# Optimization experiments

Hardware: AMD Instinct MI355X
Metric: run time of the kernel (lower is better)

The kernel has to match this reference:

```python
import jax, jax.numpy as jnp
import numpy as np

H_SIZE = 64  # height_pad == width_pad == 64 (power of 2, no padding needed)


def _hadamard(n):
    H = np.array([[1.0]], dtype=np.float32)
    while H.shape[0] < n:
        H = np.block([[H, H], [H, -H]])
    return jnp.asarray(H)


def setup_inputs() -> dict:
    key = jax.random.key(0)
    k1, k2, k3, k4 = jax.random.split(key, 4)
    B, C_in, C_out, P = 32, 256, 256, 2
    x = jax.random.normal(k1, (B, C_in, H_SIZE, H_SIZE), dtype=jnp.float32)
    v = jax.random.uniform(k2, (P, H_SIZE, H_SIZE), dtype=jnp.float32)
    W = jax.random.normal(k3, (P, C_out, C_in), dtype=jnp.float32) * (1.0 / np.sqrt(C_in))
    T = jax.random.uniform(k4, (P, H_SIZE, H_SIZE), dtype=jnp.float32) * 0.1
    return {"x": x, "v": v, "W": W, "T": T}


def reference(x, v, W, T):
    n = H_SIZE
    H = _hadamard(n)  # symmetric, H @ H = n * I
    # 2D WHT: apply along width then height
    f1 = jnp.einsum('bchw,wk->bchk', x, H)
    f2 = jnp.einsum('bchw,hk->bckw', f1, H)
    # per-pod: scale, 1x1 conv, soft-threshold
    f3 = v[:, None, None, :, :] * f2[None]                 # (p,b,c,h,w)
    f4 = jnp.einsum('poc,pbchw->pbohw', W, f3)             # 1x1 conv, no bias
    f5 = jnp.sign(f4) * jnp.maximum(jnp.abs(f4) - T[:, None, None, :, :], 0.0)
    f6 = f5.sum(axis=0)                                     # sum over pods
    # inverse 2D WHT (H^{-1} = H / n)
    f7 = jnp.einsum('bchw,wk->bchk', f6, H) / n
    f8 = jnp.einsum('bchw,hk->bckw', f7, H) / n
    return f8 + x  # residual
```

## Files before the change

### kernel.cpp

```cpp
#include <hip/hip_runtime.h>
#include <stdint.h>


typedef __attribute__((ext_vector_type(4))) float f32x4_t;
typedef __attribute__((ext_vector_type(8))) __bf16 bf16x8_t;
typedef __attribute__((ext_vector_type(8))) unsigned short u16x8_t;
typedef __attribute__((ext_vector_type(4))) unsigned short u16x4_t;

__device__ __forceinline__ float bf2f(unsigned short u) {
  union { unsigned int i; float f; } x; x.i = ((unsigned int)u) << 16; return x.f;
}
__device__ __forceinline__ unsigned short f2bf(float f) {
  union { float f; unsigned int i; } x; x.f = f;
  unsigned int i = x.i;
  return (unsigned short)((i + 0x7FFFu + ((i >> 16) & 1u)) >> 16);
}
__device__ __forceinline__ unsigned short f2bf_t(float f) {
  union { float f; unsigned int i; } x; x.f = f;
  return (unsigned short)(x.i >> 16);
}
__device__ __forceinline__ size_t Faddr(size_t f) {
  return ((f >> 12) << 13) + 4096 + (f & 4095);
}

__global__ __launch_bounds__(512) void k_fwd(const float* __restrict__ x,
                                             unsigned short* __restrict__ obuf) {
  __shared__ unsigned short smem[36864];
  int tid = threadIdx.x;
  int lane = tid & 63, wave = tid >> 6;
  int quad = lane >> 4, l15 = lane & 15;
  int cg = blockIdx.x, b = blockIdx.y;
  size_t img = (size_t)b * 256 + cg * 8 + wave;
  unsigned short* T1t = smem + wave * 4608;

  const float* xim = x + img * 4096;
#pragma unroll
  for (int l = 0; l < 16; l++) {
    int e = (l * 64 + lane) * 4;
    f32x4_t sv = *(const f32x4_t*)(xim + e);
    u16x4_t u;
#pragma unroll
    for (int j = 0; j < 4; j++) u[j] = f2bf_t(sv[j]);
    int row = e >> 6, col = e & 63;
    *(u16x4_t*)&T1t[row * 72 + col] = u;
  }

  bf16x8_t hf[2][4];
#pragma unroll
  for (int kc = 0; kc < 2; kc++)
#pragma unroll
    for (int t = 0; t < 4; t++) {
      bf16x8_t h;
#pragma unroll
      for (int j = 0; j < 8; j++) {
        int k = kc * 32 + quad * 8 + j, n = t * 16 + l15;
        h[j] = (__builtin_popcount(k & n) & 1) ? (__bf16)-1.0f : (__bf16)1.0f;
      }
      hf[kc][t] = h;
    }

  bf16x8_t xa[4][2];
#pragma unroll
  for (int mt = 0; mt < 4; mt++)
#pragma unroll
    for (int kc = 0; kc < 2; kc++)
      xa[mt][kc] = *(const bf16x8_t*)&T1t[(mt * 16 + l15) * 72 + kc * 32 + quad * 8];

#pragma unroll
  for (int nt = 0; nt < 4; nt++) {
    f32x4_t a1c[4];
#pragma unroll
    for (int mt = 0; mt < 4; mt++) a1c[mt] = (f32x4_t){0.f, 0.f, 0.f, 0.f};
#pragma unroll
    for (int kc = 0; kc < 2; kc++)
#pragma unroll
      for (int mt = 0; mt < 4; mt++)
        a1c[mt] = __builtin_amdgcn_mfma_f32_16x16x32_bf16(xa[mt][kc], hf[kc][nt], a1c[mt], 0, 0, 0);
#pragma unroll
    for (int mt = 0; mt < 4; mt++) {
      u16x4_t t4;
#pragma unroll
      for (int r = 0; r < 4; r++) t4[r] = f2bf_t(a1c[mt][r]);
      *(u16x4_t*)&T1t[(nt * 16 + l15) * 72 + mt * 16 + quad * 4] = t4;
    }
  }

  f32x4_t acc[4][4];
#pragma unroll
  for (int mt = 0; mt < 4; mt++)
#pragma unroll
    for (int nt = 0; nt < 4; nt++) acc[mt][nt] = (f32x4_t){0.f, 0.f, 0.f, 0.f};
#pragma unroll
  for (int kc = 0; kc < 2; kc++)
#pragma unroll
    for (int nt = 0; nt < 4; nt++) {
      bf16x8_t bfr = *(bf16x8_t*)&T1t[(nt * 16 + l15) * 72 + kc * 32 + quad * 8];
#pragma unroll
      for (int mt = 0; mt < 4; mt++)
        acc[mt][nt] = __builtin_amdgcn_mfma_f32_16x16x32_bf16(hf[kc][mt], bfr, acc[mt][nt], 0, 0, 0);
    }

  __syncthreads();
#pragma unroll
  for (int mt = 0; mt < 4; mt++)
#pragma unroll
    for (int nt = 0; nt < 4; nt++)
#pragma unroll
      for (int r = 0; r < 4; r++) {
        int pos = (mt * 16 + quad * 4 + r) * 64 + nt * 16 + l15;
        smem[pos * 8 + wave] = f2bf(acc[mt][nt][r]);
      }
  __syncthreads();
  size_t fbase = ((size_t)b * 32 + cg) * 4096;
#pragma unroll
  for (int i = 0; i < 8; i++) {
    int pos = i * 512 + tid;
    u16x8_t vch = *(u16x8_t*)&smem[pos * 8];
    *(u16x8_t*)(obuf + Faddr((fbase + pos) * 8)) = vch;
  }
}

__global__ __launch_bounds__(256) void k_gemm(const float* __restrict__ Wf,
                                              const float* __restrict__ vv,
                                              const float* __restrict__ TT,
                                              unsigned short* __restrict__ obuf) {
  __shared__ unsigned short smem2[24576];
  unsigned short* Alds = smem2;
  int tid = threadIdx.x;
  int lane = tid & 63, wave = tid >> 6;
  int quad = lane >> 4, l15 = lane & 15;
  int wm = wave & 1, wn = wave >> 1;
  int n0 = blockIdx.x * 128;
  int m0 = blockIdx.y * 128;
  int b  = blockIdx.z;

  f32x4_t acc[4][4];
#pragma unroll
  for (int mt = 0; mt < 4; mt++)
#pragma unroll
    for (int nt = 0; nt < 4; nt++) acc[mt][nt] = (f32x4_t){0.f, 0.f, 0.f, 0.f};

  auto issueB = [&](int ks, int buf) {
    unsigned short* Bl = smem2 + 8192 + buf * 8192;
#pragma unroll
    for (int i = 0; i < 4; i++) {
      int idx = i * 256 + tid;
      int r = idx & 127, cch = idx >> 7;
      size_t f = (((size_t)b * 32 + ks * 8 + cch) * 4096 + n0 + r) * 8;
      const unsigned short* src = obuf + Faddr(f);
      __builtin_amdgcn_global_load_lds(
          (const __attribute__((address_space(1))) void*)src,
          (__attribute__((address_space(3))) void*)(Bl + idx * 8), 16, 0, 0);
    }
  };
  auto loadA = [&](int ks, f32x4_t (&ar)[4][2]) {
    int k0 = ks * 64;
#pragma unroll
    for (int i = 0; i < 4; i++) {
      int idx = i * 256 + tid;
      int r = idx >> 3, cch = idx & 7;
      int m = m0 + r;
      const float* wp = Wf + ((m & 1) << 16) + ((m >> 1) << 8) + k0 + cch * 8;
      ar[i][0] = *(const f32x4_t*)wp;
      ar[i][1] = *(const f32x4_t*)(wp + 4);
    }
  };
  auto writeA = [&](f32x4_t (&ar)[4][2]) {
#pragma unroll
    for (int i = 0; i < 4; i++) {
      int idx = i * 256 + tid;
      int r = idx >> 3, cch = idx & 7;
      u16x8_t u;
#pragma unroll
      for (int j = 0; j < 4; j++) { u[j] = f2bf_t(ar[i][0][j]); u[4 + j] = f2bf_t(ar[i][1][j]); }
      *(u16x8_t*)&Alds[cch * 1024 + r * 8] = u;
    }
  };

  f32x4_t areg[4][2];
  issueB(0, 0);
  loadA(0, areg);
  writeA(areg);
  __syncthreads();

  int kbuf = 0;
  for (int ks = 0; ks < 4; ++ks) {
    if (ks < 3) {
      issueB(ks + 1, kbuf ^ 1);
      loadA(ks + 1, areg);
    }
    unsigned short* Bl = smem2 + 8192 + kbuf * 8192;
#pragma unroll
    for (int kk = 0; kk < 2; ++kk) {
      int ch = kk * 4 + quad;
      bf16x8_t af[4], bfr[4];
#pragma unroll
      for (int mt = 0; mt < 4; mt++)
        af[mt] = *(const bf16x8_t*)&Alds[ch * 1024 + (wm * 64 + mt * 16 + l15) * 8];
#pragma unroll
      for (int nt = 0; nt < 4; nt++)
        bfr[nt] = *(const bf16x8_t*)&Bl[ch * 1024 + (wn * 64 + nt * 16 + l15) * 8];
#pragma unroll
      for (int mt = 0; mt < 4; mt++)
#pragma unroll
        for (int nt = 0; nt < 4; nt++)
          acc[mt][nt] = __builtin_amdgcn_mfma_f32_16x16x32_bf16(af[mt], bfr[nt], acc[mt][nt], 0, 0, 0);
    }
    __syncthreads();
    if (ks < 3) {
      writeA(areg);
      __syncthreads();
    }
    kbuf ^= 1;
  }

#pragma unroll
  for (int nt = 0; nt < 4; nt++) {
    int posl = wn * 64 + nt * 16 + l15;
    int pos = n0 + posl;
    float v0 = vv[pos], v1 = vv[4096 + pos];
    float t0 = TT[pos], t1 = TT[4096 + pos];
#pragma unroll
    for (int mt = 0; mt < 4; mt++)
#pragma unroll
      for (int rp = 0; rp < 2; rp++) {
        int ol = wm * 32 + mt * 8 + quad * 2 + rp;
        float z0 = acc[mt][nt][rp * 2 + 0] * v0;
        float z1 = acc[mt][nt][rp * 2 + 1] * v1;
        float s0 = copysignf(fmaxf(fabsf(z0) - t0, 0.f), z0);
        float s1 = copysignf(fmaxf(fabsf(z1) - t1, 0.f), z1);
        smem2[ol * 136 + posl] = f2bf(s0 + s1);
      }
  }
  __syncthreads();
  int o0 = m0 >> 1;
#pragma unroll
  for (int i = 0; i < 4; i++) {
    int ci = i * 256 + tid;
    int row = ci >> 4, cc = ci & 15;
    u16x8_t vch = *(u16x8_t*)&smem2[row * 136 + cc * 8];
    size_t img = (size_t)b * 256 + o0 + row;
    *(u16x8_t*)(obuf + img * 8192 + n0 + cc * 8) = vch;
  }
}

__global__ __launch_bounds__(256) void k_inv(const float* __restrict__ x,
                                             unsigned short* __restrict__ obuf) {
  __shared__ unsigned short smem[18432];
  int tid = threadIdx.x;
  int lane = tid & 63, wave = tid >> 6;
  int quad = lane >> 4, l15 = lane & 15;
  size_t img = (size_t)blockIdx.x * 4 + wave;
  unsigned short* T1t = smem + wave * 4608;

#pragma unroll
  for (int l = 0; l < 8; l++) {
    int e = (l * 64 + lane) * 8;
    u16x8_t sv = *(const u16x8_t*)(obuf + img * 8192 + e);
    int row = e >> 6, col = e & 63;
    *(u16x8_t*)&T1t[row * 72 + col] = sv;
  }

  bf16x8_t hf[2][4];
#pragma unroll
  for (int kc = 0; kc < 2; kc++)
#pragma unroll
    for (int t = 0; t < 4; t++) {
      bf16x8_t h;
#pragma unroll
      for (int j = 0; j < 8; j++) {
        int k = kc * 32 + quad * 8 + j, n = t * 16 + l15;
        h[j] = (__builtin_popcount(k & n) & 1) ? (__bf16)-1.0f : (__bf16)1.0f;
      }
      hf[kc][t] = h;
    }

  bf16x8_t fa[4][2];
#pragma unroll
  for (int mt = 0; mt < 4; mt++)
#pragma unroll
    for (int kc = 0; kc < 2; kc++)
      fa[mt][kc] = *(const bf16x8_t*)&T1t[(mt * 16 + l15) * 72 + kc * 32 + quad * 8];

#pragma unroll
  for (int nt = 0; nt < 4; nt++) {
    f32x4_t a1c[4];
#pragma unroll
    for (int mt = 0; mt < 4; mt++) a1c[mt] = (f32x4_t){0.f, 0.f, 0.f, 0.f};
#pragma unroll
    for (int kc = 0; kc < 2; kc++)
#pragma unroll
      for (int mt = 0; mt < 4; mt++)
        a1c[mt] = __builtin_amdgcn_mfma_f32_16x16x32_bf16(fa[mt][kc], hf[kc][nt], a1c[mt], 0, 0, 0);
#pragma unroll
    for (int mt = 0; mt < 4; mt++) {
      u16x4_t t4;
#pragma unroll
      for (int r = 0; r < 4; r++) t4[r] = f2bf_t(a1c[mt][r]);
      *(u16x4_t*)&T1t[(nt * 16 + l15) * 72 + mt * 16 + quad * 4] = t4;
    }
  }

  f32x4_t acc[4][4];
#pragma unroll
  for (int mt = 0; mt < 4; mt++)
#pragma unroll
    for (int nt = 0; nt < 4; nt++) acc[mt][nt] = (f32x4_t){0.f, 0.f, 0.f, 0.f};
#pragma unroll
  for (int kc = 0; kc < 2; kc++)
#pragma unroll
    for (int nt = 0; nt < 4; nt++) {
      bf16x8_t bfr = *(bf16x8_t*)&T1t[(nt * 16 + l15) * 72 + kc * 32 + quad * 8];
#pragma unroll
      for (int mt = 0; mt < 4; mt++)
        acc[mt][nt] = __builtin_amdgcn_mfma_f32_16x16x32_bf16(hf[kc][mt], bfr, acc[mt][nt], 0, 0, 0);
    }

  const float sc = 1.0f / 4096.0f;
#pragma unroll
  for (int mt = 0; mt < 4; mt++)
#pragma unroll
    for (int nt = 0; nt < 4; nt++)
#pragma unroll
      for (int r = 0; r < 4; r++)
        T1t[(mt * 16 + quad * 4 + r) * 72 + nt * 16 + l15] = f2bf(acc[mt][nt][r] * sc);

  float* outf = (float*)obuf;
  const float* xim = x + img * 4096;
#pragma unroll
  for (int l = 0; l < 8; l++) {
    int e = (l * 64 + lane) * 8;
    int row = e >> 6, col = e & 63;
    u16x8_t tv = *(u16x8_t*)&T1t[row * 72 + col];
    f32x4_t x0 = *(const f32x4_t*)(xim + e);
    f32x4_t x1 = *(const f32x4_t*)(xim + e + 4);
    f32x4_t o0, o1;
#pragma unroll
    for (int j = 0; j < 4; j++) { o0[j] = bf2f(tv[j]) + x0[j]; o1[j] = bf2f(tv[4 + j]) + x1[j]; }
    *(f32x4_t*)(outf + img * 4096 + e) = o0;
    *(f32x4_t*)(outf + img * 4096 + e + 4) = o1;
  }
}

extern "C" void kernel_launch(void* const* d_in, const int* in_sizes, int n_in,
                              void* d_out, int out_size, void* d_ws, size_t ws_size,
                              hipStream_t stream) {
  const float* x = (const float*)d_in[0];
  const float* v = (const float*)d_in[1];
  const float* W = (const float*)d_in[2];
  const float* T = (const float*)d_in[3];
  unsigned short* obuf = (unsigned short*)d_out;
  (void)d_ws; (void)ws_size; (void)in_sizes; (void)n_in; (void)out_size;

  k_fwd<<<dim3(32, 32), 512, 0, stream>>>(x, obuf);
  k_gemm<<<dim3(32, 4, 32), 256, 0, stream>>>(W, v, T, obuf);
  k_inv<<<2048, 256, 0, stream>>>(x, obuf);
}
```

Measured before the change: 353.1 us.

## Double-buffer A tile in LDS with XOR-swizzled layout to drop a barrier

The A (weight) tile in LDS becomes double-buffered, so the next k-step's A can be written right after the MFMAs without a second __syncthreads per iteration. The A layout also changes from channel-major to row-major with an XOR swizzle on the 8-element chunk index, so row-contiguous global reads map to conflict-free LDS fragment reads. LDS use grows from 48KB to 64KB per block, which may reduce occupancy.

Result: faster. 333.5 us (-5.5%).

```diff
diff --git a/kernel.cpp b/kernel.cpp
--- a/kernel.cpp
+++ b/kernel.cpp
@@ -124,8 +124,7 @@
                                               const float* __restrict__ vv,
                                               const float* __restrict__ TT,
                                               unsigned short* __restrict__ obuf) {
-  __shared__ unsigned short smem2[24576];
-  unsigned short* Alds = smem2;
+  __shared__ unsigned short smem2[32768];
   int tid = threadIdx.x;
   int lane = tid & 63, wave = tid >> 6;
   int quad = lane >> 4, l15 = lane & 15;
@@ -141,7 +140,7 @@
     for (int nt = 0; nt < 4; nt++) acc[mt][nt] = (f32x4_t){0.f, 0.f, 0.f, 0.f};
 
   auto issueB = [&](int ks, int buf) {
-    unsigned short* Bl = smem2 + 8192 + buf * 8192;
+    unsigned short* Bl = smem2 + 16384 + buf * 8192;
 #pragma unroll
     for (int i = 0; i < 4; i++) {
       int idx = i * 256 + tid;
@@ -153,50 +152,55 @@
           (__attribute__((address_space(3))) void*)(Bl + idx * 8), 16, 0, 0);
     }
   };
-  auto loadA = [&](int ks, f32x4_t (&ar)[4][2]) {
+  auto fetchA = [&](int ks, f32x4_t (&ar)[4][2]) {
     int k0 = ks * 64;
 #pragma unroll
     for (int i = 0; i < 4; i++) {
       int idx = i * 256 + tid;
       int r = idx >> 3, cch = idx & 7;
+      int gch = cch ^ (r & 7);
       int m = m0 + r;
-      const float* wp = Wf + ((m & 1) << 16) + ((m >> 1) << 8) + k0 + cch * 8;
+      const float* wp = Wf + ((m & 1) << 16) + ((m >> 1) << 8) + k0 + gch * 8;
       ar[i][0] = *(const f32x4_t*)wp;
       ar[i][1] = *(const f32x4_t*)(wp + 4);
     }
   };
-  auto writeA = [&](f32x4_t (&ar)[4][2]) {
+  auto writeA = [&](int buf, f32x4_t (&ar)[4][2]) {
+    unsigned short* Al = smem2 + buf * 8192;
 #pragma unroll
     for (int i = 0; i < 4; i++) {
       int idx = i * 256 + tid;
-      int r = idx >> 3, cch = idx & 7;
       u16x8_t u;
 #pragma unroll
       for (int j = 0; j < 4; j++) { u[j] = f2bf_t(ar[i][0][j]); u[4 + j] = f2bf_t(ar[i][1][j]); }
-      *(u16x8_t*)&Alds[cch * 1024 + r * 8] = u;
+      *(u16x8_t*)&Al[idx * 8] = u;
     }
   };
 
   f32x4_t areg[4][2];
   issueB(0, 0);
-  loadA(0, areg);
-  writeA(areg);
+  fetchA(0, areg);
+  writeA(0, areg);
   __syncthreads();
 
-  int kbuf = 0;
   for (int ks = 0; ks < 4; ++ks) {
+    int p = ks & 1;
     if (ks < 3) {
-      issueB(ks + 1, kbuf ^ 1);
-      loadA(ks + 1, areg);
-    }
-    unsigned short* Bl = smem2 + 8192 + kbuf * 8192;
+      issueB(ks + 1, p ^ 1);
+      fetchA(ks + 1, areg);
+    }
+    unsigned short* Al = smem2 + p * 8192;
+    unsigned short* Bl = smem2 + 16384 + p * 8192;
 #pragma unroll
     for (int kk = 0; kk < 2; ++kk) {
+      bf16x8_t af[4], bfr[4];
+#pragma unroll
+      for (int mt = 0; mt < 4; mt++) {
+        int row = wm * 64 + mt * 16 + l15;
+        int s = (kk * 4 + quad) ^ (row & 7);
+        af[mt] = *(const bf16x8_t*)&Al[row * 64 + s * 8];
+      }
       int ch = kk * 4 + quad;
-      bf16x8_t af[4], bfr[4];
-#pragma unroll
-      for (int mt = 0; mt < 4; mt++)
-        af[mt] = *(const bf16x8_t*)&Alds[ch * 1024 + (wm * 64 + mt * 16 + l15) * 8];
 #pragma unroll
       for (int nt = 0; nt < 4; nt++)
         bfr[nt] = *(const bf16x8_t*)&Bl[ch * 1024 + (wn * 64 + nt * 16 + l15) * 8];
@@ -206,12 +210,8 @@
         for (int nt = 0; nt < 4; nt++)
           acc[mt][nt] = __builtin_amdgcn_mfma_f32_16x16x32_bf16(af[mt], bfr[nt], acc[mt][nt], 0, 0, 0);
     }
+    if (ks < 3) writeA(p ^ 1, areg);
     __syncthreads();
-    if (ks < 3) {
-      writeA(areg);
-      __syncthreads();
-    }
-    kbuf ^= 1;
   }
 
 #pragma unroll
```
